# Kernel optimization log

Hardware: AMD Instinct MI355X
Metric: run time of the kernel (lower is better)

The kernel has to match this reference:

```python
import jax, jax.numpy as jnp
import numpy as np

N_VARS = 8192
N_CHECKS = 4096
DC = 6          # check degree (edges per check)
DV = 3          # variable degree
N_EDGES = N_CHECKS * DC  # == N_VARS * DV == 24576
NUM_ITERS = 5
BATCH = 2048


def setup_inputs() -> dict:
    key = jax.random.key(0)
    k1, _ = jax.random.split(key)
    channel_llrs = jax.random.normal(k1, (BATCH, N_VARS), dtype=jnp.float32)
    # Regular Tanner graph: edges sorted by check (constant degree DC),
    # variable side is a random permutation with each var appearing DV times.
    H_rows = jnp.asarray(np.repeat(np.arange(N_CHECKS), DC), dtype=jnp.int32)
    rng = np.random.default_rng(0)
    H_cols = jnp.asarray(rng.permutation(np.repeat(np.arange(N_VARS), DV)), dtype=jnp.int32)
    weights = jnp.full((NUM_ITERS, 1), 0.5, dtype=jnp.float32)  # nn.Parameter init
    return {"channel_llrs": channel_llrs, "weights": weights,
            "H_rows": H_rows, "H_cols": H_cols, "n_checks": N_CHECKS}


def _decode(channel_llrs, weights, H_cols, n_checks):
    B, n_vars = channel_llrs.shape
    E = H_cols.shape[0]
    dc = E // n_checks  # constant check degree (edges sorted by check)
    pos = jnp.arange(dc)
    c2v = jnp.zeros((B, E), dtype=channel_llrs.dtype)
    for i in range(weights.shape[0]):
        # variable-node update: sum incoming c2v per variable, exclude self edge
        agg = jnp.zeros((B, n_vars), dtype=channel_llrs.dtype).at[:, H_cols].add(c2v)
        var_llrs = channel_llrs + agg
        v2c = var_llrs[:, H_cols] - c2v                      # [B, E]
        # check-node update (min-sum with self-exclusion), grouped per check
        g = v2c.reshape(B, n_checks, dc)                     # [B, C, dc]
        s = jnp.sign(g)
        prod_s = jnp.prod(s, axis=-1, keepdims=True)
        s_in = jnp.where(s == 0, 1.0, s)                     # torch: sign_in[sign_in==0]=1
        out_sign = prod_s / s_in
        a = jnp.abs(g)
        amin = jnp.min(a, axis=-1, keepdims=True)
        imin = jnp.argmin(a, axis=-1, keepdims=True)
        a2 = jnp.where(pos == imin, jnp.inf, a)
        min2 = jnp.min(a2, axis=-1, keepdims=True)
        min_others = jnp.where(pos == imin, min2, amin)      # min over all-but-self
        c2v = (out_sign * min_others).reshape(B, E) * weights[i]
    final_agg = jnp.zeros((B, n_vars), dtype=channel_llrs.dtype).at[:, H_cols].add(c2v)
    return channel_llrs + final_agg


def reference(channel_llrs, weights, H_rows, H_cols, n_checks):
    # H_rows == repeat(arange(n_checks), dc) by construction; grouping is done
    # via the [n_checks, dc] reshape (same partition as the original per-check loop).
    return _decode(channel_llrs, weights, H_cols, n_checks)
```

## Files before the change

kernel.cpp:

```cpp
#include <hip/hip_runtime.h>
#include <stdint.h>

#define NV    8192
#define NC    4096
#define DC    6
#define DV    3
#define NE    24576
#define NITER 5
#define BATCH 2048


__global__ void build_v2e(const int* __restrict__ cols, int* __restrict__ cnt,
                          unsigned short* __restrict__ v2e_tmp) {
  int e = blockIdx.x * blockDim.x + threadIdx.x;
  if (e >= NE) return;
  int v = cols[e];
  int s = atomicAdd(&cnt[v], 1);
  v2e_tmp[v * DV + s] = (unsigned short)e;
}

__global__ void invert_slots(const unsigned short* __restrict__ v2e_tmp,
                             unsigned short* __restrict__ cslot) {
  int v = blockIdx.x * blockDim.x + threadIdx.x;
  if (v >= NV) return;
  int a = v2e_tmp[v * 3 + 0];
  int b = v2e_tmp[v * 3 + 1];
  int c = v2e_tmp[v * 3 + 2];
  int t;
  if (a > b) { t = a; a = b; b = t; }
  if (b > c) { t = b; b = c; c = t; }
  if (a > b) { t = a; a = b; b = t; }
  cslot[a] = (unsigned short)(0 * NV + v);
  cslot[b] = (unsigned short)(1 * NV + v);
  cslot[c] = (unsigned short)(2 * NV + v);
}


__global__ __launch_bounds__(64) void greedy_schedule(
    const unsigned short* __restrict__ cslot, unsigned int* __restrict__ slotp) {
  __shared__ unsigned short sl[64][6];
  __shared__ unsigned short pm[64][6];
  __shared__ int cnt[32];

  const int l = threadIdx.x;
  const int c = blockIdx.x * 64 + l;

  const unsigned int* cs32 = (const unsigned int*)cslot;
  unsigned int a0 = cs32[c * 3 + 0];
  unsigned int a1 = cs32[c * 3 + 1];
  unsigned int a2 = cs32[c * 3 + 2];
  sl[l][0] = (unsigned short)(a0 & 0xffffu); sl[l][1] = (unsigned short)(a0 >> 16);
  sl[l][2] = (unsigned short)(a1 & 0xffffu); sl[l][3] = (unsigned short)(a1 >> 16);
  sl[l][4] = (unsigned short)(a2 & 0xffffu); sl[l][5] = (unsigned short)(a2 >> 16);

  unsigned int used = 0;
  for (int j = 0; j < 6; ++j) {
    if (l < 32) cnt[l] = 0;
    __syncthreads();
    int placed = -1;
    for (int k = 0; k < 6; ++k) {
      if (placed >= 0) break;
      if (used & (1u << k)) continue;
      int bk = sl[l][k] & 31;
      int old = atomicAdd(&cnt[bk], 1);
      if (old < 2) placed = k;
      else atomicSub(&cnt[bk], 1);
    }
    if (placed < 0) {
      for (int k = 0; k < 6; ++k)
        if (!(used & (1u << k))) { placed = k; break; }
    }
    used |= (1u << placed);
    pm[l][j] = sl[l][placed];
    __syncthreads();
  }

  slotp[0 * NC + c] = (unsigned int)pm[l][0] | ((unsigned int)pm[l][1] << 16);
  slotp[1 * NC + c] = (unsigned int)pm[l][2] | ((unsigned int)pm[l][3] << 16);
  slotp[2 * NC + c] = (unsigned int)pm[l][4] | ((unsigned int)pm[l][5] << 16);
}


__global__ __launch_bounds__(1024) void decode_kernel(
    const float* __restrict__ ch, const float* __restrict__ wts,
    const unsigned int* __restrict__ slotp, float* __restrict__ out) {
  __shared__ float s_msg[NE];

  const int tid = threadIdx.x;
  const int b = blockIdx.x;
  const float* chrow = ch + (size_t)b * NV;
  const float4* ch4 = (const float4*)chrow;

  float4 chreg[2];
  chreg[0] = ch4[tid];
  chreg[1] = ch4[1024 + tid];

  float w[NITER];
#pragma unroll
  for (int i = 0; i < NITER; ++i) w[i] = wts[i];

  int idx[4][6];
#pragma unroll
  for (int r = 0; r < 4; ++r) {
    int c = tid + r * 1024;
    unsigned int p0 = slotp[c];
    unsigned int p1 = slotp[NC + c];
    unsigned int p2 = slotp[2 * NC + c];
    idx[r][0] = (int)(p0 & 0xFFFFu); idx[r][1] = (int)(p0 >> 16);
    idx[r][2] = (int)(p1 & 0xFFFFu); idx[r][3] = (int)(p1 >> 16);
    idx[r][4] = (int)(p2 & 0xFFFFu); idx[r][5] = (int)(p2 >> 16);
  }

  float4* m0 = (float4*)&s_msg[0];
  float4* m1 = (float4*)&s_msg[NV];
  float4* m2 = (float4*)&s_msg[2 * NV];

#pragma unroll
  for (int p = 0; p < 2; ++p) {
    int i4 = p * 1024 + tid;
    float4 v = chreg[p];
    m0[i4] = v; m1[i4] = v; m2[i4] = v;
  }
  __syncthreads();

  for (int it = 0; it < NITER; ++it) {
    const float wi = w[it];

#pragma unroll
    for (int r = 0; r < 4; ++r) {
      unsigned int u[6];
      float m1v = INFINITY, m2v = INFINITY;
      unsigned int xs = 0u;
#pragma unroll
      for (int j = 0; j < 6; ++j) {
        float t = s_msg[idx[r][j]];
        unsigned int uu = __float_as_uint(t);
        u[j] = uu;
        xs ^= uu;
        float a = fabsf(t);
        m2v = fminf(m2v, fmaxf(m1v, a));
        m1v = fminf(m1v, a);
      }
      const bool anyz = (m1v == 0.0f);
      const float m1w = m1v * wi;
      const float m2w = m2v * wi;
#pragma unroll
      for (int j = 0; j < 6; ++j) {
        float a = __uint_as_float(u[j] & 0x7FFFFFFFu);
        float mag = (a == m1v) ? m2w : m1w;
        unsigned int s = (xs ^ u[j]) & 0x80000000u;
        float o = __uint_as_float(__float_as_uint(mag) ^ s);
        if (anyz) o = 0.0f;
        s_msg[idx[r][j]] = o;
      }
    }
    __syncthreads();

    if (it < NITER - 1) {
#pragma unroll
      for (int p = 0; p < 2; ++p) {
        int i4 = p * 1024 + tid;
        float4 c0 = m0[i4], c1 = m1[i4], c2 = m2[i4];
        float4 cr = chreg[p];
        float4 vl;
        vl.x = cr.x + ((c0.x + c1.x) + c2.x);
        vl.y = cr.y + ((c0.y + c1.y) + c2.y);
        vl.z = cr.z + ((c0.z + c1.z) + c2.z);
        vl.w = cr.w + ((c0.w + c1.w) + c2.w);
        float4 o0 = {vl.x - c0.x, vl.y - c0.y, vl.z - c0.z, vl.w - c0.w};
        float4 o1 = {vl.x - c1.x, vl.y - c1.y, vl.z - c1.z, vl.w - c1.w};
        float4 o2 = {vl.x - c2.x, vl.y - c2.y, vl.z - c2.z, vl.w - c2.w};
        m0[i4] = o0; m1[i4] = o1; m2[i4] = o2;
      }
      __syncthreads();
    }
  }

  float4* orow4 = (float4*)(out + (size_t)b * NV);
#pragma unroll
  for (int p = 0; p < 2; ++p) {
    int i4 = p * 1024 + tid;
    float4 c0 = m0[i4], c1 = m1[i4], c2 = m2[i4];
    float4 cr = chreg[p];
    float4 o;
    o.x = cr.x + ((c0.x + c1.x) + c2.x);
    o.y = cr.y + ((c0.y + c1.y) + c2.y);
    o.z = cr.z + ((c0.z + c1.z) + c2.z);
    o.w = cr.w + ((c0.w + c1.w) + c2.w);
    orow4[i4] = o;
  }
}


extern "C" void kernel_launch(void* const* d_in, const int* in_sizes, int n_in,
                              void* d_out, int out_size, void* d_ws, size_t ws_size,
                              hipStream_t stream) {
  (void)in_sizes; (void)n_in; (void)out_size; (void)ws_size;

  const float* ch   = (const float*)d_in[0];
  const float* wts  = (const float*)d_in[1];
  const int*  Hcols = (const int*)d_in[3];
  float* out = (float*)d_out;

  char* ws = (char*)d_ws;
  int*            cnt     = (int*)(ws + 0);
  unsigned short* v2e_tmp = (unsigned short*)(ws + 32768);
  unsigned short* cslot   = (unsigned short*)(ws + 81920);
  unsigned int*   slotp   = (unsigned int*)(ws + 131072);

  hipMemsetAsync(cnt, 0, NV * sizeof(int), stream);
  build_v2e<<<(NE + 255) / 256, 256, 0, stream>>>(Hcols, cnt, v2e_tmp);
  invert_slots<<<(NV + 255) / 256, 256, 0, stream>>>(v2e_tmp, cslot);
  greedy_schedule<<<NC / 64, 64, 0, stream>>>(cslot, slotp);

  decode_kernel<<<BATCH, 1024, 0, stream>>>(ch, wts, slotp, out);
}
```

Baseline: 150.6 us.

## Refine check-edge schedule with per-step bank counts and pairwise swap passes

The greedy scheduler now keeps a separate LDS bank-occupancy count for each of the six gather steps and starts its search at a rotated position per lane. It then runs local-search passes that swap step assignments within a check whenever that lowers an estimated bank-conflict cost. The goal is fewer LDS bank conflicts in the decode kernel's indexed shared-memory gathers and scatters. The decode kernel's variable-update pass also switches from float4 to float2 shared accesses, which may change bank conflicts on the ds_read/ds_write vectors but doubles the instruction count.

```diff
diff --git a/kernel.cpp b/kernel.cpp
--- a/kernel.cpp
+++ b/kernel.cpp
@@ -36,11 +36,15 @@
 }
 
 
+__device__ __forceinline__ int icost(int n) {
+  return (n > 2) ? (((n + 1) >> 1) - 1) : 0;
+}
+
 __global__ __launch_bounds__(64) void greedy_schedule(
     const unsigned short* __restrict__ cslot, unsigned int* __restrict__ slotp) {
   __shared__ unsigned short sl[64][6];
-  __shared__ unsigned short pm[64][6];
-  __shared__ int cnt[32];
+  __shared__ unsigned char perm[64][6];
+  __shared__ int cnt[6][32];
 
   const int l = threadIdx.x;
   const int c = blockIdx.x * 64 + l;
@@ -53,31 +57,57 @@
   sl[l][2] = (unsigned short)(a1 & 0xffffu); sl[l][3] = (unsigned short)(a1 >> 16);
   sl[l][4] = (unsigned short)(a2 & 0xffffu); sl[l][5] = (unsigned short)(a2 >> 16);
 
+  for (int t = l; t < 192; t += 64) ((int*)cnt)[t] = 0;
+  __syncthreads();
+
   unsigned int used = 0;
   for (int j = 0; j < 6; ++j) {
-    if (l < 32) cnt[l] = 0;
-    __syncthreads();
     int placed = -1;
-    for (int k = 0; k < 6; ++k) {
-      if (placed >= 0) break;
+    for (int kk = 0; kk < 6; ++kk) {
+      int k = (kk + l + j) % 6;
       if (used & (1u << k)) continue;
       int bk = sl[l][k] & 31;
-      int old = atomicAdd(&cnt[bk], 1);
-      if (old < 2) placed = k;
-      else atomicSub(&cnt[bk], 1);
+      int old = atomicAdd(&cnt[j][bk], 1);
+      if (old < 2) { placed = k; break; }
+      atomicSub(&cnt[j][bk], 1);
     }
     if (placed < 0) {
       for (int k = 0; k < 6; ++k)
         if (!(used & (1u << k))) { placed = k; break; }
+      atomicAdd(&cnt[j][sl[l][placed] & 31], 1);
     }
     used |= (1u << placed);
-    pm[l][j] = sl[l][placed];
+    perm[l][j] = (unsigned char)placed;
     __syncthreads();
   }
 
-  slotp[0 * NC + c] = (unsigned int)pm[l][0] | ((unsigned int)pm[l][1] << 16);
-  slotp[1 * NC + c] = (unsigned int)pm[l][2] | ((unsigned int)pm[l][3] << 16);
-  slotp[2 * NC + c] = (unsigned int)pm[l][4] | ((unsigned int)pm[l][5] << 16);
+  for (int pass = 0; pass < 4; ++pass) {
+    for (int j1 = 0; j1 < 6; ++j1) {
+      for (int j2 = j1 + 1; j2 < 6; ++j2) {
+        int k1 = perm[l][j1], k2 = perm[l][j2];
+        int b1 = sl[l][k1] & 31, b2 = sl[l][k2] & 31;
+        if (b1 != b2) {
+          int c11 = cnt[j1][b1], c12 = cnt[j1][b2];
+          int c21 = cnt[j2][b1], c22 = cnt[j2][b2];
+          int dOld = icost(c11) + icost(c12) + icost(c21) + icost(c22);
+          int dNew = icost(c11 - 1) + icost(c12 + 1) + icost(c22 - 1) + icost(c21 + 1);
+          if (dNew < dOld) {
+            atomicSub(&cnt[j1][b1], 1); atomicAdd(&cnt[j1][b2], 1);
+            atomicSub(&cnt[j2][b2], 1); atomicAdd(&cnt[j2][b1], 1);
+            perm[l][j1] = (unsigned char)k2; perm[l][j2] = (unsigned char)k1;
+          }
+        }
+        __syncthreads();
+      }
+    }
+  }
+
+  unsigned short pm[6];
+#pragma unroll
+  for (int j = 0; j < 6; ++j) pm[j] = sl[l][perm[l][j]];
+  slotp[0 * NC + c] = (unsigned int)pm[0] | ((unsigned int)pm[1] << 16);
+  slotp[1 * NC + c] = (unsigned int)pm[2] | ((unsigned int)pm[3] << 16);
+  slotp[2 * NC + c] = (unsigned int)pm[4] | ((unsigned int)pm[5] << 16);
 }
 
 
@@ -88,12 +118,11 @@
 
   const int tid = threadIdx.x;
   const int b = blockIdx.x;
-  const float* chrow = ch + (size_t)b * NV;
-  const float4* ch4 = (const float4*)chrow;
-
-  float4 chreg[2];
-  chreg[0] = ch4[tid];
-  chreg[1] = ch4[1024 + tid];
+  const float2* ch2 = (const float2*)(ch + (size_t)b * NV);
+
+  float2 chreg[4];
+#pragma unroll
+  for (int p = 0; p < 4; ++p) chreg[p] = ch2[tid + p * 1024];
 
   float w[NITER];
 #pragma unroll
@@ -111,15 +140,15 @@
     idx[r][4] = (int)(p2 & 0xFFFFu); idx[r][5] = (int)(p2 >> 16);
   }
 
-  float4* m0 = (float4*)&s_msg[0];
-  float4* m1 = (float4*)&s_msg[NV];
-  float4* m2 = (float4*)&s_msg[2 * NV];
-
-#pragma unroll
-  for (int p = 0; p < 2; ++p) {
-    int i4 = p * 1024 + tid;
-    float4 v = chreg[p];
-    m0[i4] = v; m1[i4] = v; m2[i4] = v;
+  float2* m0 = (float2*)&s_msg[0];
+  float2* m1 = (float2*)&s_msg[NV];
+  float2* m2 = (float2*)&s_msg[2 * NV];
+
+#pragma unroll
+  for (int p = 0; p < 4; ++p) {
+    int i2 = p * 1024 + tid;
+    float2 v = chreg[p];
+    m0[i2] = v; m1[i2] = v; m2[i2] = v;
   }
   __syncthreads();
 
@@ -158,36 +187,32 @@
 
     if (it < NITER - 1) {
 #pragma unroll
-      for (int p = 0; p < 2; ++p) {
-        int i4 = p * 1024 + tid;
-        float4 c0 = m0[i4], c1 = m1[i4], c2 = m2[i4];
-        float4 cr = chreg[p];
-        float4 vl;
+      for (int p = 0; p < 4; ++p) {
+        int i2 = p * 1024 + tid;
+        float2 c0 = m0[i2], c1 = m1[i2], c2 = m2[i2];
+        float2 cr = chreg[p];
+        float2 vl;
         vl.x = cr.x + ((c0.x + c1.x) + c2.x);
         vl.y = cr.y + ((c0.y + c1.y) + c2.y);
-        vl.z = cr.z + ((c0.z + c1.z) + c2.z);
-        vl.w = cr.w + ((c0.w + c1.w) + c2.w);
-        float4 o0 = {vl.x - c0.x, vl.y - c0.y, vl.z - c0.z, vl.w - c0.w};
-        float4 o1 = {vl.x - c1.x, vl.y - c1.y, vl.z - c1.z, vl.w - c1.w};
-        float4 o2 = {vl.x - c2.x, vl.y - c2.y, vl.z - c2.z, vl.w - c2.w};
-        m0[i4] = o0; m1[i4] = o1; m2[i4] = o2;
+        float2 o0 = {vl.x - c0.x, vl.y - c0.y};
+        float2 o1 = {vl.x - c1.x, vl.y - c1.y};
+        float2 o2 = {vl.x - c2.x, vl.y - c2.y};
+        m0[i2] = o0; m1[i2] = o1; m2[i2] = o2;
       }
       __syncthreads();
     }
   }
 
-  float4* orow4 = (float4*)(out + (size_t)b * NV);
-#pragma unroll
-  for (int p = 0; p < 2; ++p) {
-    int i4 = p * 1024 + tid;
-    float4 c0 = m0[i4], c1 = m1[i4], c2 = m2[i4];
-    float4 cr = chreg[p];
-    float4 o;
+  float2* orow2 = (float2*)(out + (size_t)b * NV);
+#pragma unroll
+  for (int p = 0; p < 4; ++p) {
+    int i2 = p * 1024 + tid;
+    float2 c0 = m0[i2], c1 = m1[i2], c2 = m2[i2];
+    float2 cr = chreg[p];
+    float2 o;
     o.x = cr.x + ((c0.x + c1.x) + c2.x);
     o.y = cr.y + ((c0.y + c1.y) + c2.y);
-    o.z = cr.z + ((c0.z + c1.z) + c2.z);
-    o.w = cr.w + ((c0.w + c1.w) + c2.w);
-    orow4[i4] = o;
+    orow2[i2] = o;
   }
 }
 
```

Measured after the change: 176.6 us. 17.2% more time.

## Schedule check edge order per quarter-wave to cut LDS bank conflicts

Applied to the files above, without the earlier changes.

The greedy scheduler that orders each check's six shared-memory message slots now balances banks per 16-lane group and per slot position j, rather than per whole block with a limit of two. It starts from a rotated greedy assignment and then runs pairwise swap refinement passes that reduce excess bank collisions. The aim is fewer LDS bank conflicts on the gather and scatter accesses in the decode kernel. The setup kernel does more work with many barriers, but it runs once and is small.

```diff
diff --git a/kernel.cpp b/kernel.cpp
--- a/kernel.cpp
+++ b/kernel.cpp
@@ -36,13 +36,16 @@
 }
 
 
+__device__ __forceinline__ int qc(int n) { return (n > 1) ? (n - 1) : 0; }
+
 __global__ __launch_bounds__(64) void greedy_schedule(
     const unsigned short* __restrict__ cslot, unsigned int* __restrict__ slotp) {
   __shared__ unsigned short sl[64][6];
-  __shared__ unsigned short pm[64][6];
-  __shared__ int cnt[32];
+  __shared__ unsigned char perm[64][6];
+  __shared__ int cnt[6][4][32];
 
   const int l = threadIdx.x;
+  const int q = l >> 4;
   const int c = blockIdx.x * 64 + l;
 
   const unsigned int* cs32 = (const unsigned int*)cslot;
@@ -53,31 +56,64 @@
   sl[l][2] = (unsigned short)(a1 & 0xffffu); sl[l][3] = (unsigned short)(a1 >> 16);
   sl[l][4] = (unsigned short)(a2 & 0xffffu); sl[l][5] = (unsigned short)(a2 >> 16);
 
+  for (int t = l; t < 6 * 4 * 32; t += 64) ((int*)cnt)[t] = 0;
+  __syncthreads();
+
   unsigned int used = 0;
   for (int j = 0; j < 6; ++j) {
-    if (l < 32) cnt[l] = 0;
-    __syncthreads();
     int placed = -1;
-    for (int k = 0; k < 6; ++k) {
-      if (placed >= 0) break;
+    for (int kk = 0; kk < 6; ++kk) {
+      int k = (kk + l) % 6;
       if (used & (1u << k)) continue;
       int bk = sl[l][k] & 31;
-      int old = atomicAdd(&cnt[bk], 1);
-      if (old < 2) placed = k;
-      else atomicSub(&cnt[bk], 1);
+      if (atomicAdd(&cnt[j][q][bk], 1) == 0) { placed = k; break; }
+      atomicSub(&cnt[j][q][bk], 1);
     }
     if (placed < 0) {
-      for (int k = 0; k < 6; ++k)
-        if (!(used & (1u << k))) { placed = k; break; }
+      int bc = 1 << 30;
+      for (int k = 0; k < 6; ++k) {
+        if (used & (1u << k)) continue;
+        int cc = cnt[j][q][sl[l][k] & 31];
+        if (cc < bc) { bc = cc; placed = k; }
+      }
+      atomicAdd(&cnt[j][q][sl[l][placed] & 31], 1);
     }
     used |= (1u << placed);
-    pm[l][j] = sl[l][placed];
+    perm[l][j] = (unsigned char)placed;
     __syncthreads();
   }
 
-  slotp[0 * NC + c] = (unsigned int)pm[l][0] | ((unsigned int)pm[l][1] << 16);
-  slotp[1 * NC + c] = (unsigned int)pm[l][2] | ((unsigned int)pm[l][3] << 16);
-  slotp[2 * NC + c] = (unsigned int)pm[l][4] | ((unsigned int)pm[l][5] << 16);
+  for (int pass = 0; pass < 4; ++pass) {
+    for (int s = 0; s < 2; ++s) {
+      for (int j1 = 0; j1 < 6; ++j1) {
+        for (int j2 = j1 + 1; j2 < 6; ++j2) {
+          if ((l & 1) == s) {
+            int k1 = perm[l][j1], k2 = perm[l][j2];
+            int b1 = sl[l][k1] & 31, b2 = sl[l][k2] & 31;
+            if (b1 != b2) {
+              int c11 = cnt[j1][q][b1], c12 = cnt[j1][q][b2];
+              int c21 = cnt[j2][q][b1], c22 = cnt[j2][q][b2];
+              int dOld = qc(c11) + qc(c12) + qc(c21) + qc(c22);
+              int dNew = qc(c11 - 1) + qc(c12 + 1) + qc(c21 + 1) + qc(c22 - 1);
+              if (dNew < dOld) {
+                atomicSub(&cnt[j1][q][b1], 1); atomicAdd(&cnt[j1][q][b2], 1);
+                atomicSub(&cnt[j2][q][b2], 1); atomicAdd(&cnt[j2][q][b1], 1);
+                perm[l][j1] = (unsigned char)k2; perm[l][j2] = (unsigned char)k1;
+              }
+            }
+          }
+          __syncthreads();
+        }
+      }
+    }
+  }
+
+  unsigned short pm[6];
+#pragma unroll
+  for (int j = 0; j < 6; ++j) pm[j] = sl[l][perm[l][j]];
+  slotp[0 * NC + c] = (unsigned int)pm[0] | ((unsigned int)pm[1] << 16);
+  slotp[1 * NC + c] = (unsigned int)pm[2] | ((unsigned int)pm[3] << 16);
+  slotp[2 * NC + c] = (unsigned int)pm[4] | ((unsigned int)pm[5] << 16);
 }
 
 
```

After: 162.4 us. 7.8% more time.
